# Optimization experiments

Hardware: AMD Instinct MI355X
Metric: run time of the kernel (lower is better)

The kernel has to match this reference:

```python
import jax, jax.numpy as jnp
import numpy as np

DEPTH = 4
N_MOLS = 2000
ATOMS_PER_MOL = 50
N_ATOMS = N_MOLS * ATOMS_PER_MOL + 1   # +1 zero-padding row (chemprop convention)
N_BONDS = 200001                        # +1 zero-padding row
MAX_NB = 6
ATOM_FDIM, BOND_FDIM, HIDDEN = 133, 147, 300


def setup_inputs() -> dict:
    key = jax.random.key(0)
    ks = jax.random.split(key, 12)
    f_atoms = jax.random.uniform(ks[0], (N_ATOMS, ATOM_FDIM), jnp.float32).at[0].set(0.0)
    f_bonds = jax.random.uniform(ks[1], (N_BONDS, BOND_FDIM), jnp.float32).at[0].set(0.0)
    w_atoms = jax.random.uniform(ks[2], (N_ATOMS,), jnp.float32) + 0.5
    w_bonds = (jax.random.uniform(ks[3], (N_BONDS,), jnp.float32) + 0.5).at[0].set(0.0)
    a2b = jax.random.randint(ks[4], (N_ATOMS, MAX_NB), 0, N_BONDS, jnp.int32)
    b2a = jax.random.randint(ks[5], (N_BONDS,), 0, N_ATOMS, jnp.int32)
    b2revb = jax.random.randint(ks[6], (N_BONDS,), 0, N_BONDS, jnp.int32)
    # segment id per atom; padding atom 0 -> dummy segment N_MOLS (dropped)
    mol_id = jnp.concatenate([jnp.array([N_MOLS], jnp.int32),
                              jnp.repeat(jnp.arange(N_MOLS, dtype=jnp.int32), ATOMS_PER_MOL)])
    degree_of_polym = jax.random.uniform(ks[7], (N_MOLS,), jnp.float32) + 0.5
    s = 0.05
    W_i = jax.random.normal(ks[8], (BOND_FDIM, HIDDEN), jnp.float32) * s
    W_h = jax.random.normal(ks[9], (HIDDEN, HIDDEN), jnp.float32) * s
    W_o = jax.random.normal(ks[10], (ATOM_FDIM + HIDDEN, HIDDEN), jnp.float32) * s
    b_o = jnp.zeros((HIDDEN,), jnp.float32)
    return dict(f_atoms=f_atoms, f_bonds=f_bonds, w_atoms=w_atoms, w_bonds=w_bonds,
                degree_of_polym=degree_of_polym, W_i=W_i, W_h=W_h, W_o=W_o, b_o=b_o,
                a2b=a2b, b2a=b2a, b2revb=b2revb, mol_id=mol_id)


def reference(f_atoms, f_bonds, w_atoms, w_bonds, degree_of_polym,
              W_i, W_h, W_o, b_o, a2b, b2a, b2revb, mol_id):
    # bond-message MPNN (atom_messages=False, undirected=False, ReLU, dropout=0 eval)
    inp = f_bonds @ W_i                                   # [n_bonds, H], no bias
    message = jax.nn.relu(inp)
    for _ in range(DEPTH - 1):
        # gather incoming directed-bond messages per atom and weight them
        nei_msg = message[a2b] * w_bonds[a2b][..., None]  # [n_atoms, max_nb, H]
        a_message = nei_msg.sum(axis=1)                   # [n_atoms, H]
        # subtract reverse message (weighted)
        message = a_message[b2a] - message[b2revb] * w_bonds[:, None]
        message = jax.nn.relu(inp + message @ W_h)
    # final atom aggregation
    nei_msg = message[a2b] * w_bonds[a2b][..., None]
    a_message = nei_msg.sum(axis=1)                       # [n_atoms, H]
    a_input = jnp.concatenate([f_atoms, a_message], axis=1)
    atom_hiddens = jax.nn.relu(a_input @ W_o + b_o)       # [n_atoms, H]
    # per-molecule weighted mean readout, scaled by degree of polymerization
    weighted = w_atoms[:, None] * atom_hiddens
    sums = jax.ops.segment_sum(weighted, mol_id, num_segments=N_MOLS + 1)[:N_MOLS]
    wsum = jax.ops.segment_sum(w_atoms, mol_id, num_segments=N_MOLS + 1)[:N_MOLS]
    mol_vecs = degree_of_polym[:, None] * (sums / wsum[:, None])
    return mol_vecs
```

## Files before the change

### kernel.cpp

```cpp
#include <hip/hip_runtime.h>

#define N_MOLS  2000
#define APM     50
#define N_ATOMS 100001
#define N_BONDS 200001
#define MAX_NB  6
#define AF      133
#define BF      147
#define H       300

#define SB    304
#define SF    152
#define MB_P  200064
#define MA_P  100096
#define SWH   320
#define SWI   160
#define SWO   480

typedef _Float16 f16x8 __attribute__((ext_vector_type(8)));
typedef float    f32x4 __attribute__((ext_vector_type(4)));

__device__ inline unsigned int f32_to_fp8(float f) {
    union { _Float16 h; unsigned short u; } cv; cv.h = (_Float16)f;
    const unsigned short u = cv.u;
    const int s = (u >> 15) & 1;
    const int e = (u >> 10) & 31;
    const int m = u & 1023;
    int e8 = e - 8;
    if (e8 <= 0) return s << 7;
    int m8 = (m + 64) >> 7;
    if (m8 == 8) { m8 = 0; e8 += 1; }
    if (e8 > 15 || (e8 == 15 && m8 > 6)) return (s << 7) | 0x7E;
    return (s << 7) | (e8 << 3) | m8;
}
__device__ inline float fp8_to_f32(unsigned int c) {
    const int s = (c >> 7) & 1, e = (c >> 3) & 15, m = c & 7;
    if (e == 0) return 0.f;
    union { unsigned short u; _Float16 h; } cv;
    cv.u = (unsigned short)((s << 15) | ((e + 8) << 10) | (m << 7));
    return (float)cv.h;
}

__global__ void cast_fb_kernel(const float* __restrict__ src, _Float16* __restrict__ dst) {
    unsigned i = blockIdx.x * blockDim.x + threadIdx.x;
    if (i >= (unsigned)MB_P * SF) return;
    unsigned m = i / SF, k = i % SF;
    dst[i] = (_Float16)((m < N_BONDS && k < BF) ? src[(size_t)m * BF + k] : 0.f);
}
__global__ void cast_fa_kernel(const float* __restrict__ src, _Float16* __restrict__ dst) {
    unsigned i = blockIdx.x * blockDim.x + threadIdx.x;
    if (i >= (unsigned)MA_P * SF) return;
    unsigned m = i / SF, k = i % SF;
    dst[i] = (_Float16)((m < N_ATOMS && k < AF) ? src[(size_t)m * AF + k] : 0.f);
}
__global__ void cast_wh_kernel(const float* __restrict__ W, _Float16* __restrict__ Wt) {
    int i = blockIdx.x * blockDim.x + threadIdx.x;
    if (i >= 320 * SWH) return;
    int n = i / SWH, k = i % SWH;
    Wt[i] = (_Float16)((n < H && k < H) ? W[k * H + n] : 0.f);
}
__global__ void cast_wi_kernel(const float* __restrict__ W, _Float16* __restrict__ Wt) {
    int i = blockIdx.x * blockDim.x + threadIdx.x;
    if (i >= 320 * SWI) return;
    int n = i / SWI, k = i % SWI;
    Wt[i] = (_Float16)((n < H && k < BF) ? W[k * H + n] : 0.f);
}
__global__ void cast_wo_kernel(const float* __restrict__ W, _Float16* __restrict__ Wt) {
    int i = blockIdx.x * blockDim.x + threadIdx.x;
    if (i >= 320 * SWO) return;
    int n = i / SWO, r = i % SWO;
    float v = 0.f;
    if (n < H) {
        if (r < 320) { if (r < H) v = W[(AF + r) * H + n]; }
        else         { int rr = r - 320; if (rr < AF) v = W[rr * H + n]; }
    }
    Wt[i] = (_Float16)v;
}

template<int NCHUNK, int MODE>
__global__ __launch_bounds__(256, 3) void dgemm_kernel(
    const _Float16* __restrict__ A1, const _Float16* __restrict__ A2,
    const _Float16* __restrict__ Wt, const float* __restrict__ bias,
    _Float16* __restrict__ out16, unsigned char* __restrict__ out8)
{
    __shared__ _Float16 Bs[320 * 40];
    const int tid  = threadIdx.x;
    const int lane = tid & 63, wave = tid >> 6;
    const int r16  = lane & 15, quad = lane >> 4;
    const int rh   = wave >> 1, ch = wave & 1;
    const int row0 = blockIdx.x * 64 + rh * 32 + r16;
    const int colbase = ch * 160;
    constexpr int SW = (MODE == 0) ? SWI : (MODE == 1 ? SWH : SWO);

    f32x4 acc[2][10];
    #pragma unroll
    for (int s = 0; s < 2; ++s)
        #pragma unroll
        for (int ct = 0; ct < 10; ++ct) acc[s][ct] = f32x4{0.f, 0.f, 0.f, 0.f};

    #pragma unroll 1
    for (int kc = 0; kc < NCHUNK; ++kc) {
        __syncthreads();
        for (int n = tid; n < 320; n += 256) {
            const _Float16* src = Wt + (size_t)n * SW + kc * 32;
            f16x8 t0 = *(const f16x8*)(src + 0);
            f16x8 t1 = *(const f16x8*)(src + 8);
            f16x8 t2 = *(const f16x8*)(src + 16);
            f16x8 t3 = *(const f16x8*)(src + 24);
            *(f16x8*)(&Bs[n * 40 + 0])  = t0;
            *(f16x8*)(&Bs[n * 40 + 8])  = t1;
            *(f16x8*)(&Bs[n * 40 + 16]) = t2;
            *(f16x8*)(&Bs[n * 40 + 24]) = t3;
        }
        __syncthreads();

        const _Float16* ap; int kl, sa;
        if (MODE == 2 && kc >= 10) { ap = A2; kl = kc - 10; sa = SF; }
        else                       { ap = A1; kl = kc; sa = (MODE == 0 ? SF : SB); }
        const f16x8 a0 = *(const f16x8*)(ap + (size_t)row0 * sa + kl * 32 + quad * 8);
        const f16x8 a1 = *(const f16x8*)(ap + (size_t)(row0 + 16) * sa + kl * 32 + quad * 8);
        #pragma unroll
        for (int ct = 0; ct < 10; ++ct) {
            const f16x8 b = *(const f16x8*)(&Bs[(colbase + ct * 16 + r16) * 40 + quad * 8]);
            acc[0][ct] = __builtin_amdgcn_mfma_f32_16x16x32_f16(a0, b, acc[0][ct], 0, 0, 0);
            acc[1][ct] = __builtin_amdgcn_mfma_f32_16x16x32_f16(a1, b, acc[1][ct], 0, 0, 0);
        }
    }

    const int rowb = blockIdx.x * 64 + rh * 32 + quad * 4;
    #pragma unroll
    for (int ct = 0; ct < 10; ++ct) {
        const int col = colbase + ct * 16 + r16;
        if (col >= SB) continue;
        const float bv = (MODE == 2 && col < H) ? bias[col] : 0.f;
        #pragma unroll
        for (int s = 0; s < 2; ++s) {
            #pragma unroll
            for (int e = 0; e < 4; ++e) {
                const int row = rowb + s * 16 + e;
                const float v = acc[s][ct][e] + bv;
                if (MODE == 0) {
                    out8 [(size_t)row * SB + col] = (unsigned char)f32_to_fp8(v);
                    out16[(size_t)row * SB + col] = (_Float16)(v > 0.f ? v : 0.f);
                } else if (MODE == 1) {
                    out16[(size_t)row * SB + col] = (_Float16)v;
                } else {
                    out16[(size_t)row * SB + col] = (_Float16)(v > 0.f ? v : 0.f);
                }
            }
        }
    }
}

__global__ __launch_bounds__(256, 8) void aggregate_kernel(
    const _Float16* __restrict__ src,
    const int* __restrict__ a2b,
    const float* __restrict__ w_bonds,
    _Float16* __restrict__ dst)
{
    const int lane = threadIdx.x & 63;
    const int a = blockIdx.x * 4 + (threadIdx.x >> 6);
    if (a >= N_ATOMS || lane >= 38) return;
    const int h0 = lane * 8;
    float acc[8] = {0, 0, 0, 0, 0, 0, 0, 0};
    #pragma unroll
    for (int k = 0; k < MAX_NB; ++k) {
        const int b = a2b[a * MAX_NB + k];
        const float w = w_bonds[b];
        const f16x8 m = *(const f16x8*)(src + (size_t)b * SB + h0);
        #pragma unroll
        for (int j = 0; j < 8; ++j) acc[j] += w * (float)m[j];
    }
    f16x8 o;
    #pragma unroll
    for (int j = 0; j < 8; ++j) o[j] = (_Float16)acc[j];
    *(f16x8*)(dst + (size_t)a * SB + h0) = o;
}

__global__ __launch_bounds__(256, 8) void update_kernel(
    const unsigned char* __restrict__ inp8,
    const _Float16* __restrict__ hm,
    const _Float16* __restrict__ hb,
    const int* __restrict__ b2a,
    const int* __restrict__ b2revb,
    const float* __restrict__ w_bonds,
    _Float16* __restrict__ msg)
{
    const int lane = threadIdx.x & 63;
    const int b = blockIdx.x * 4 + (threadIdx.x >> 6);
    if (b >= MB_P || lane >= 38) return;
    const bool real = b < N_BONDS;
    const int bc = real ? b : 0;
    const int a  = b2a[bc];
    const int rb = b2revb[bc];
    const float w = w_bonds[bc];
    const int h0 = lane * 8;
    const uint2 i8  = *(const uint2*)(inp8 + (size_t)b * SB + h0);
    const f16x8 hmv = *(const f16x8*)(hm + (size_t)a  * SB + h0);
    const f16x8 hbv = *(const f16x8*)(hb + (size_t)rb * SB + h0);
    f16x8 o;
    #pragma unroll
    for (int j = 0; j < 8; ++j) {
        const unsigned int c = ((j < 4 ? i8.x : i8.y) >> (8 * (j & 3))) & 255u;
        const float v = fp8_to_f32(c) + (float)hmv[j] - w * (float)hbv[j];
        o[j] = (_Float16)((real && v > 0.f) ? v : 0.f);
    }
    *(f16x8*)(msg + (size_t)b * SB + h0) = o;
}

__global__ __launch_bounds__(256, 8) void readout_kernel(
    const _Float16* __restrict__ ah,
    const float* __restrict__ w_atoms,
    const float* __restrict__ dop,
    float* __restrict__ out)
{
    const int lane = threadIdx.x & 63;
    const int m = blockIdx.x * 4 + (threadIdx.x >> 6);
    if (m >= N_MOLS || lane >= 38) return;
    const int h0 = lane * 8;
    const int a0 = 1 + m * APM;
    float acc[8] = {0, 0, 0, 0, 0, 0, 0, 0};
    float wsum = 0.f;
    for (int i = 0; i < APM; ++i) {
        const float w = w_atoms[a0 + i];
        wsum += w;
        const f16x8 v = *(const f16x8*)(ah + (size_t)(a0 + i) * SB + h0);
        #pragma unroll
        for (int j = 0; j < 8; ++j) acc[j] += w * (float)v[j];
    }
    const float s = dop[m] / wsum;
    #pragma unroll
    for (int j = 0; j < 8; ++j) {
        const int h = h0 + j;
        if (h < H) out[(size_t)m * H + h] = s * acc[j];
    }
}

extern "C" void kernel_launch(void* const* d_in, const int* in_sizes, int n_in,
                              void* d_out, int out_size, void* d_ws, size_t ws_size,
                              hipStream_t stream) {
    const float* f_atoms = (const float*)d_in[0];
    const float* f_bonds = (const float*)d_in[1];
    const float* w_atoms = (const float*)d_in[2];
    const float* w_bonds = (const float*)d_in[3];
    const float* dop     = (const float*)d_in[4];
    const float* W_i     = (const float*)d_in[5];
    const float* W_h     = (const float*)d_in[6];
    const float* W_o     = (const float*)d_in[7];
    const float* b_o     = (const float*)d_in[8];
    const int* a2b    = (const int*)d_in[9];
    const int* b2a    = (const int*)d_in[10];
    const int* b2revb = (const int*)d_in[11];
    float* out = (float*)d_out;

    char* p = (char*)d_ws;
    auto alloc = [&](size_t bytes) {
        char* q = p;
        p += ((bytes + 64  + 255) / 256) * 256;
        return q;
    };
    unsigned char* inp8 = (unsigned char*)alloc((size_t)MB_P * SB);
    _Float16* msg  = (_Float16*)alloc((size_t)MB_P * SB * 2);
    _Float16* hb   = (_Float16*)alloc((size_t)MB_P * SB * 2);
    _Float16* hm   = (_Float16*)alloc((size_t)MA_P * SB * 2);
    _Float16* Wth  = (_Float16*)alloc((size_t)320 * SWH * 2);
    _Float16* Wti  = (_Float16*)alloc((size_t)320 * SWI * 2);
    _Float16* Wto  = (_Float16*)alloc((size_t)320 * SWO * 2);
    _Float16* fb16 = hb;
    _Float16* fa16 = (_Float16*)inp8;
    _Float16* ah   = hb;

    if ((size_t)(p - (char*)d_ws) > ws_size) {
        hipMemsetAsync(d_out, 0, (size_t)out_size * sizeof(float), stream);
        return;
    }

    {
        unsigned n1 = (unsigned)MB_P * SF;
        cast_fb_kernel<<<(n1 + 255) / 256, 256, 0, stream>>>(f_bonds, fb16);
        cast_wh_kernel<<<(320 * SWH + 255) / 256, 256, 0, stream>>>(W_h, Wth);
        cast_wi_kernel<<<(320 * SWI + 255) / 256, 256, 0, stream>>>(W_i, Wti);
        cast_wo_kernel<<<(320 * SWO + 255) / 256, 256, 0, stream>>>(W_o, Wto);
    }

    const int gB = MB_P / 64;
    const int gA = MA_P / 64;
    const int aggGrid = (N_ATOMS + 3) / 4;
    const int updGrid = MB_P / 4;

    dgemm_kernel<5, 0><<<gB, 256, 0, stream>>>(fb16, nullptr, Wti, nullptr, msg, inp8);
    for (int d = 0; d < 3; ++d) {
        dgemm_kernel<10, 1><<<gB, 256, 0, stream>>>(msg, nullptr, Wth, nullptr, hb, nullptr);
        aggregate_kernel<<<aggGrid, 256, 0, stream>>>(hb, a2b, w_bonds, hm);
        update_kernel<<<updGrid, 256, 0, stream>>>(inp8, hm, hb, b2a, b2revb, w_bonds, msg);
    }
    aggregate_kernel<<<aggGrid, 256, 0, stream>>>(msg, a2b, w_bonds, hm);
    {
        unsigned n2 = (unsigned)MA_P * SF;
        cast_fa_kernel<<<(n2 + 255) / 256, 256, 0, stream>>>(f_atoms, fa16);
    }
    dgemm_kernel<15, 2><<<gA, 256, 0, stream>>>(hm, fa16, Wto, b_o, ah, nullptr);
    readout_kernel<<<(N_MOLS + 3) / 4, 256, 0, stream>>>(ah, w_atoms, dop, out);
}
```

Baseline: 1.351 ms.

## Keep full-K weight slice resident in LDS and enlarge per-wave row tile

The GEMM kernel now loads the whole K extent of a 160-column weight half into shared memory once per block, instead of restaging a 32-wide K chunk with two barriers per iteration. Each wave computes a 64-row by 160-column tile (4x10 MFMA accumulators), and blocks are split into tile/half pairs. This removes the per-chunk synchronisation and raises MFMA work per LDS read of B. In exchange it uses more registers and LDS, which lowers occupancy (launch bounds drop to 1), and the A rows are reloaded twice, once per column half. Bond padding is rounded up to a multiple of 256 to match the new tile.

```diff
diff --git a/kernel.cpp b/kernel.cpp
--- a/kernel.cpp
+++ b/kernel.cpp
@@ -11,7 +11,7 @@
 
 #define SB    304
 #define SF    152
-#define MB_P  200064
+#define MB_P  200192
 #define MA_P  100096
 #define SWH   320
 #define SWI   160
@@ -78,74 +78,75 @@
 }
 
 template<int NCHUNK, int MODE>
-__global__ __launch_bounds__(256, 3) void dgemm_kernel(
+__global__ __launch_bounds__(256, 1) void dgemm_kernel(
     const _Float16* __restrict__ A1, const _Float16* __restrict__ A2,
     const _Float16* __restrict__ Wt, const float* __restrict__ bias,
     _Float16* __restrict__ out16, unsigned char* __restrict__ out8)
 {
-    __shared__ _Float16 Bs[320 * 40];
+    constexpr int K   = NCHUNK * 32;
+    constexpr int STR = K + 8;
+    constexpr int KC8 = K / 8;
+    constexpr int SW  = (MODE == 0) ? SWI : (MODE == 1 ? SWH : SWO);
+    __shared__ __align__(16) _Float16 Bs[160 * STR];
+
     const int tid  = threadIdx.x;
     const int lane = tid & 63, wave = tid >> 6;
     const int r16  = lane & 15, quad = lane >> 4;
-    const int rh   = wave >> 1, ch = wave & 1;
-    const int row0 = blockIdx.x * 64 + rh * 32 + r16;
-    const int colbase = ch * 160;
-    constexpr int SW = (MODE == 0) ? SWI : (MODE == 1 ? SWH : SWO);
-
-    f32x4 acc[2][10];
-    #pragma unroll
-    for (int s = 0; s < 2; ++s)
+    const int tile = blockIdx.x >> 1, half = blockIdx.x & 1;
+    const int colbase = half * 160;
+
+    for (int idx = tid; idx < 160 * KC8; idx += 256) {
+        const int c  = idx / KC8;
+        const int kk = (idx - c * KC8) * 8;
+        *(f16x8*)(&Bs[c * STR + kk]) = *(const f16x8*)(Wt + (size_t)(colbase + c) * SW + kk);
+    }
+    __syncthreads();
+
+    const int row0 = tile * 256 + wave * 64;
+
+    f32x4 acc[4][10];
+    #pragma unroll
+    for (int s = 0; s < 4; ++s)
         #pragma unroll
         for (int ct = 0; ct < 10; ++ct) acc[s][ct] = f32x4{0.f, 0.f, 0.f, 0.f};
 
-    #pragma unroll 1
+    #pragma unroll
     for (int kc = 0; kc < NCHUNK; ++kc) {
-        __syncthreads();
-        for (int n = tid; n < 320; n += 256) {
-            const _Float16* src = Wt + (size_t)n * SW + kc * 32;
-            f16x8 t0 = *(const f16x8*)(src + 0);
-            f16x8 t1 = *(const f16x8*)(src + 8);
-            f16x8 t2 = *(const f16x8*)(src + 16);
-            f16x8 t3 = *(const f16x8*)(src + 24);
-            *(f16x8*)(&Bs[n * 40 + 0])  = t0;
-            *(f16x8*)(&Bs[n * 40 + 8])  = t1;
-            *(f16x8*)(&Bs[n * 40 + 16]) = t2;
-            *(f16x8*)(&Bs[n * 40 + 24]) = t3;
-        }
-        __syncthreads();
-
         const _Float16* ap; int kl, sa;
         if (MODE == 2 && kc >= 10) { ap = A2; kl = kc - 10; sa = SF; }
         else                       { ap = A1; kl = kc; sa = (MODE == 0 ? SF : SB); }
-        const f16x8 a0 = *(const f16x8*)(ap + (size_t)row0 * sa + kl * 32 + quad * 8);
-        const f16x8 a1 = *(const f16x8*)(ap + (size_t)(row0 + 16) * sa + kl * 32 + quad * 8);
+        f16x8 a[4];
+        #pragma unroll
+        for (int s = 0; s < 4; ++s)
+            a[s] = *(const f16x8*)(ap + (size_t)(row0 + s * 16 + r16) * sa + kl * 32 + quad * 8);
         #pragma unroll
         for (int ct = 0; ct < 10; ++ct) {
-            const f16x8 b = *(const f16x8*)(&Bs[(colbase + ct * 16 + r16) * 40 + quad * 8]);
-            acc[0][ct] = __builtin_amdgcn_mfma_f32_16x16x32_f16(a0, b, acc[0][ct], 0, 0, 0);
-            acc[1][ct] = __builtin_amdgcn_mfma_f32_16x16x32_f16(a1, b, acc[1][ct], 0, 0, 0);
+            const f16x8 b = *(const f16x8*)(&Bs[(ct * 16 + r16) * STR + kc * 32 + quad * 8]);
+            #pragma unroll
+            for (int s = 0; s < 4; ++s)
+                acc[s][ct] = __builtin_amdgcn_mfma_f32_16x16x32_f16(a[s], b, acc[s][ct], 0, 0, 0);
         }
     }
 
-    const int rowb = blockIdx.x * 64 + rh * 32 + quad * 4;
     #pragma unroll
     for (int ct = 0; ct < 10; ++ct) {
         const int col = colbase + ct * 16 + r16;
         if (col >= SB) continue;
         const float bv = (MODE == 2 && col < H) ? bias[col] : 0.f;
         #pragma unroll
-        for (int s = 0; s < 2; ++s) {
+        for (int s = 0; s < 4; ++s) {
+            const int rowb = row0 + s * 16 + quad * 4;
             #pragma unroll
             for (int e = 0; e < 4; ++e) {
-                const int row = rowb + s * 16 + e;
                 const float v = acc[s][ct][e] + bv;
+                const size_t off = (size_t)(rowb + e) * SB + col;
                 if (MODE == 0) {
-                    out8 [(size_t)row * SB + col] = (unsigned char)f32_to_fp8(v);
-                    out16[(size_t)row * SB + col] = (_Float16)(v > 0.f ? v : 0.f);
+                    out8 [off] = (unsigned char)f32_to_fp8(v);
+                    out16[off] = (_Float16)(v > 0.f ? v : 0.f);
                 } else if (MODE == 1) {
-                    out16[(size_t)row * SB + col] = (_Float16)v;
+                    out16[off] = (_Float16)v;
                 } else {
-                    out16[(size_t)row * SB + col] = (_Float16)(v > 0.f ? v : 0.f);
+                    out16[off] = (_Float16)(v > 0.f ? v : 0.f);
                 }
             }
         }
@@ -283,8 +284,8 @@
         cast_wo_kernel<<<(320 * SWO + 255) / 256, 256, 0, stream>>>(W_o, Wto);
     }
 
-    const int gB = MB_P / 64;
-    const int gA = MA_P / 64;
+    const int gB = (MB_P / 256) * 2;
+    const int gA = (MA_P / 256) * 2;
     const int aggGrid = (N_ATOMS + 3) / 4;
     const int updGrid = MB_P / 4;
 
```

After: 1.461 ms. 1.08x slower.
